# Optimization experiments

Hardware: AMD Instinct MI355X
Metric: run time of the kernel (lower is better)

## Reference

```python
import jax, jax.numpy as jnp
import numpy as np

B, FIN, N, K, FOUT = 8, 64, 2048, 20, 128
BN_EPS = 1e-5
LEAKY_SLOPE = 0.01


def _conv2d(x, w, b):
    # x: [B,C,H,W], w: [O,I,kh,kw] -> valid conv, stride 1
    y = jax.lax.conv_general_dilated(
        x, w, window_strides=(1, 1), padding='VALID',
        dimension_numbers=('NCHW', 'OIHW', 'NCHW'))
    return y + b[None, :, None, None]


def _batchnorm(x, gamma, beta):
    # training-mode BN: batch stats over (B,H,W), biased variance (torch default)
    mean = jnp.mean(x, axis=(0, 2, 3), keepdims=True)
    var = jnp.var(x, axis=(0, 2, 3), keepdims=True)
    xn = (x - mean) * jax.lax.rsqrt(var + BN_EPS)
    return xn * gamma[None, :, None, None] + beta[None, :, None, None]


def _edge_features(x, k):
    # x: [B, D, N] -> [B, 2D, N, k]
    xt = jnp.transpose(x, (0, 2, 1))                      # [B,N,D]
    sq = jnp.sum(xt * xt, axis=-1)                        # [B,N]
    dist = sq[:, :, None] + sq[:, None, :] - 2.0 * jnp.einsum('bnd,bmd->bnm', xt, xt)
    # smallest k+1 distances (self is the smallest); drop self
    _, idx = jax.lax.top_k(-dist, k + 1)                  # [B,N,k+1]
    idx = idx[:, :, 1:]                                   # [B,N,k]
    nb = jax.vmap(lambda pts, ind: pts[ind])(xt, idx)     # [B,N,k,D]
    neighbors = jnp.transpose(nb, (0, 3, 1, 2))           # [B,D,N,k]
    central = x[:, :, :, None]                            # [B,D,N,1]
    central_k = jnp.broadcast_to(central, neighbors.shape)
    return jnp.concatenate([central_k, neighbors - central], axis=1)


def setup_inputs() -> dict:
    key = jax.random.key(0)
    ks = jax.random.split(key, 4)
    x = jax.random.normal(ks[0], (B, FIN, N), dtype=jnp.float32)
    conv1_w = jax.random.normal(ks[1], (4 * FIN, 2 * FIN, 1, K // 2 + 1), dtype=jnp.float32) * 0.02
    conv1_b = jnp.zeros((4 * FIN,), jnp.float32)
    bn1_g = jnp.ones((4 * FIN,), jnp.float32)
    bn1_b = jnp.zeros((4 * FIN,), jnp.float32)
    conv2_w = jax.random.normal(ks[2], (2 * FOUT, 2 * FIN, 1, 2 * K), dtype=jnp.float32) * 0.02
    conv2_b = jnp.zeros((2 * FOUT,), jnp.float32)
    bn2_g = jnp.ones((2 * FOUT,), jnp.float32)
    bn2_b = jnp.zeros((2 * FOUT,), jnp.float32)
    return {"x": x, "conv1_w": conv1_w, "conv1_b": conv1_b, "bn1_g": bn1_g,
            "bn1_b": bn1_b, "conv2_w": conv2_w, "conv2_b": conv2_b,
            "bn2_g": bn2_g, "bn2_b": bn2_b, "k": K}


def reference(x, conv1_w, conv1_b, bn1_g, bn1_b, conv2_w, conv2_b, bn2_g, bn2_b, k):
    ee = _edge_features(x, k)                             # [B,2Fin,N,k]
    Bb, CC, NN, KK = ee.shape
    # inte_conv_hk: conv [1, k//2+1] -> [B,4Fin,N,k/2], BN, LeakyReLU
    h = _batchnorm(_conv2d(ee, conv1_w, conv1_b), bn1_g, bn1_b)
    h = jnp.where(h > 0, h, LEAKY_SLOPE * h)
    # transpose/view dance: [B,N,4Fin,k/2] -> [B,N,2Fin,k] -> [B,2Fin,N,k]
    inte = jnp.transpose(h, (0, 2, 1, 3)).reshape(Bb, NN, CC, KK)
    inte = jnp.transpose(inte, (0, 2, 1, 3))
    merge = jnp.concatenate([ee, inte], axis=3)           # [B,2Fin,N,2k]
    y = _batchnorm(_conv2d(merge, conv2_w, conv2_b), bn2_g, bn2_b)
    y = jax.nn.relu(y)                                    # [B,2Fout,N,1]
    fout = y.shape[1] // 2
    return y.reshape(Bb, fout, 2 * NN)                    # [B,Fout,2N]
```

## Files before the change

### kernel.cpp

```cpp
#include <hip/hip_runtime.h>
#include <stdint.h>

typedef unsigned int uint;
typedef unsigned short ushort;
typedef __attribute__((ext_vector_type(8))) short short8;
typedef __attribute__((ext_vector_type(4))) float f32x4;

__device__ __forceinline__ uint f2bf(float f) {
  uint u = __float_as_uint(f);
  return (u + 0x7fffu + ((u >> 16) & 1u)) >> 16;
}
__device__ __forceinline__ float bf2f(uint us) {
  return __uint_as_float(us << 16);
}
__device__ __forceinline__ uint cvtpk_bf16(float lo, float hi) {
  uint r;
  asm("v_cvt_pk_bf16_f32 %0, %1, %2" : "=v"(r) : "v"(lo), "v"(hi));
  return r;
}
__device__ __forceinline__ int lt_count(unsigned long long m) {
  return (int)__builtin_amdgcn_mbcnt_hi((uint)(m >> 32),
             __builtin_amdgcn_mbcnt_lo((uint)m, 0u));
}

__global__ __launch_bounds__(256) void prep_transpose(
    const float* __restrict__ w1, const float* __restrict__ w2,
    ushort* __restrict__ wp1, ushort* __restrict__ wpack,
    const float* __restrict__ x, uint* __restrict__ xtu,
    float* __restrict__ xtf, float* __restrict__ sqf) {
  __shared__ float t[64][65];
  int tid = threadIdx.x;
  if (blockIdx.x >= 256) {
    int g = (blockIdx.x - 256) * 256 + tid;
    if (g < 196608) {
      int chunk = g >> 9;
      int r = g & 511;
      int lane = r >> 3, j = r & 7;
      int tks = chunk >> 4;
      int ctile = chunk & 15;
      int tt0 = tks >> 1, ks = tks & 1;
      int c = ctile * 16 + (lane & 15);
      int d = ks * 32 + ((lane >> 4) << 3) + j;
      float val;
      if (tt0 < 11) {
        val = w1[c * 1408 + (64 + d) * 11 + tt0];
      } else {
        float s = 0.f;
        for (int tt = 0; tt < 11; ++tt)
          s += w1[c * 1408 + d * 11 + tt] - w1[c * 1408 + (64 + d) * 11 + tt];
        val = s;
      }
      wp1[g] = (ushort)f2bf(val);
    } else {
      int gp = g - 196608;
      int chunk = gp >> 9;
      int r = gp & 511;
      int lane = r >> 3, j = r & 7;
      int kb = chunk >> 5;
      int rem = chunk & 31;
      int ks = rem >> 4, ctile = rem & 15;
      int c = ctile * 16 + (lane & 15);
      int k = kb * 64 + ks * 32 + ((lane >> 4) << 3) + j;
      float val;
      if (k < 64) {
        int d = k;
        float s = 0.f;
        for (int jn = 0; jn < 20; ++jn)
          s += w2[c * 5120 + d * 40 + jn] - w2[c * 5120 + (64 + d) * 40 + jn];
        val = s;
      } else if (k < 1344) {
        int q = k - 64; int jn = q >> 6, d = q & 63;
        val = w2[c * 5120 + (64 + d) * 40 + jn];
      } else {
        int q = k - 1344; int ci = q / 20, jj = q - ci * 20;
        val = w2[c * 5120 + ci * 40 + 20 + jj];
      }
      wpack[gp] = (ushort)f2bf(val);
    }
    return;
  }
  int blk = blockIdx.x;
  int b = blk >> 5, n0 = (blk & 31) << 6;
  const float* xb = x + b * 131072;
  #pragma unroll
  for (int it = 0; it < 16; ++it) {
    int d = (it << 2) + (tid >> 6);
    int n = tid & 63;
    t[d][n] = xb[d * 2048 + n0 + n];
  }
  __syncthreads();
  #pragma unroll
  for (int it = 0; it < 8; ++it) {
    int n = (it << 3) + (tid >> 5);
    int dp = tid & 31;
    float f0 = t[2 * dp][n], f1 = t[2 * dp + 1][n];
    uint v = f2bf(f0) | (f2bf(f1) << 16);
    size_t col = (size_t)(b * 2048 + n0 + n);
    xtu[col * 32 + dp] = v;
    float2 fv; fv.x = f0; fv.y = f1;
    *(float2*)&xtf[(col << 6) + 2 * dp] = fv;
    float s = f0 * f0 + f1 * f1;
    #pragma unroll
    for (int off = 16; off > 0; off >>= 1) s += __shfl_xor(s, off);
    if (dp == 0) sqf[col] = s;
  }
}

__global__ __launch_bounds__(1024) void knn_kernel(
    const ushort* __restrict__ xbf_t, const float* __restrict__ sqf,
    int* __restrict__ cbuf) {
  __shared__ uint dist[16][1040];
  __shared__ uint surv[16][132];
  int tid = threadIdx.x;
  int wv = tid >> 6, lane = tid & 63;
  int grp = blockIdx.x >> 1;
  int half = blockIdx.x & 1;
  int cbase = half << 10;
  int row0 = grp << 4;
  int b = row0 >> 11, n0 = row0 & 2047;
  const ushort* xt = xbf_t + ((size_t)b << 17);
  const float* sqb = sqf + (b << 11);
  int m = lane & 15, quad = lane >> 4;
  short8 afr0 = *(const short8*)(xt + ((size_t)(n0 + m) << 6) + quad * 8);
  short8 afr1 = *(const short8*)(xt + ((size_t)(n0 + m) << 6) + 32 + quad * 8);
  for (int t = 0; t < 4; ++t) {
    int lcol = (((wv << 2) + t) << 4) + m;
    int col = cbase + lcol;
    short8 bfr0 = *(const short8*)(xt + ((size_t)col << 6) + quad * 8);
    short8 bfr1 = *(const short8*)(xt + ((size_t)col << 6) + 32 + quad * 8);
    f32x4 c = {};
    c = __builtin_amdgcn_mfma_f32_16x16x32_bf16(afr0, bfr0, c, 0, 0, 0);
    c = __builtin_amdgcn_mfma_f32_16x16x32_bf16(afr1, bfr1, c, 0, 0, 0);
    float sq = sqb[col];
    #pragma unroll
    for (int r = 0; r < 4; ++r) {
      float f = sq - 2.f * c[r];
      uint u = __float_as_uint(f);
      uint srt = u ^ ((uint)((int)u >> 31) | 0x80000000u);
      dist[quad * 4 + r][lcol] = (srt & 0xFFFFF800u) | (uint)col;
    }
  }
  __syncthreads();
  uint* dr = dist[wv];
  int selfl = (n0 + wv) - cbase;
  if (selfl >= 0 && selfl < 1024 && ((selfl & 63) == lane))
    dr[selfl] = 0xFFFFFFFFu;

  uint key[16];
  uint v0 = 0xFFFFFFFFu;
  #pragma unroll
  for (int l = 0; l < 16; ++l) {
    uint v = dr[(l << 6) + lane];
    key[l] = v;
    v0 = v0 < v ? v0 : v;
  }

  uint s = v0;
  #pragma unroll
  for (int k = 2; k <= 64; k <<= 1) {
    #pragma unroll
    for (int j = k >> 1; j > 0; j >>= 1) {
      uint o = (uint)__shfl_xor((int)s, j);
      bool up = ((lane & k) == 0);
      bool lower = ((lane & j) == 0);
      uint mn = s < o ? s : o;
      uint mx = s < o ? o : s;
      s = (lower == up) ? mn : mx;
    }
  }
  uint T = (uint)__shfl((int)s, 31);

  int base = 0;
  #pragma unroll
  for (int l = 0; l < 16; ++l) {
    uint v = key[l];
    bool f = (v <= T);
    unsigned long long mk = __ballot(f);
    if (f) {
      int pos = base + lt_count(mk);
      if (pos < 128) surv[wv][pos] = v;
    }
    base += __popcll(mk);
  }
  int S = base < 128 ? base : 128;
  if (lane < 4) surv[wv][S + lane] = 0xFFFFFFFFu;

  int outb = (row0 + wv) * 64 + (half << 5);
  uint k0 = (lane < S) ? surv[wv][lane] : 0xFFFFFFFFu;
  int r0 = 0;
  if (S > 64) {
    uint k1 = (lane + 64 < S) ? surv[wv][lane + 64] : 0xFFFFFFFFu;
    int r1 = 0;
    for (int i = 0; i < S; i += 4) {
      uint4 q = *(const uint4*)&surv[wv][i];
      r0 += (q.x < k0) + (q.y < k0) + (q.z < k0) + (q.w < k0);
      r1 += (q.x < k1) + (q.y < k1) + (q.z < k1) + (q.w < k1);
    }
    if (lane + 64 < S && r1 < 32) cbuf[outb + r1] = (int)(k1 & 2047u);
  } else {
    for (int i = 0; i < S; i += 4) {
      uint4 q = *(const uint4*)&surv[wv][i];
      r0 += (q.x < k0) + (q.y < k0) + (q.z < k0) + (q.w < k0);
    }
  }
  if (lane < S && r0 < 32) cbuf[outb + r0] = (int)(k0 & 2047u);
}

__global__ __launch_bounds__(256) void knn_merge(
    const float* __restrict__ xtf, const int* __restrict__ cbuf,
    int* __restrict__ idxout) {
  __shared__ double dkey[4][64];
  __shared__ int ccol[4][64];
  int tid = threadIdx.x;
  int wv = tid >> 6, lane = tid & 63;
  int row = (blockIdx.x << 2) + wv;
  int b = row >> 11, n = row & 2047;
  int ci = cbuf[row * 64 + lane];
  const float* xc = xtf + ((size_t)b << 17);
  const float4* xj4 = (const float4*)(xc + ((size_t)ci << 6));
  const float4* xi4 = (const float4*)(xc + ((size_t)n << 6));
  double dt = 0.0, s2 = 0.0;
  #pragma unroll 4
  for (int d4 = 0; d4 < 16; ++d4) {
    float4 vj = xj4[d4];
    float4 vi = xi4[d4];
    double a0 = (double)vj.x, a1 = (double)vj.y, a2 = (double)vj.z, a3 = (double)vj.w;
    s2 += a0 * a0 + a1 * a1 + a2 * a2 + a3 * a3;
    dt += (double)vi.x * a0 + (double)vi.y * a1 + (double)vi.z * a2 + (double)vi.w * a3;
  }
  dkey[wv][lane] = s2 - 2.0 * dt;
  ccol[wv][lane] = ci;
  __syncthreads();
  double kl = dkey[wv][lane];
  int rank = 0;
  for (int mm = 0; mm < 64; ++mm) {
    double km = dkey[wv][mm];
    int cm = ccol[wv][mm];
    if (km < kl || (km == kl && cm < ci)) ++rank;
  }
  if (rank < 20) idxout[row * 20 + rank] = ci;
}

__global__ __launch_bounds__(512, 4) void conv1_mfma(
    const ushort* __restrict__ xbf_t, const int* __restrict__ idxbuf,
    const ushort* __restrict__ wp1, uint* __restrict__ hu,
    float* __restrict__ stats) {
  __shared__ ushort sl[21][8][16][8];
  __shared__ int nidx[16][20];
  int tid = threadIdx.x;
  int p0 = blockIdx.x << 4;
  int b = p0 >> 11, n0 = p0 & 2047;
  const ushort* xt = xbf_t + ((size_t)b << 17);
  for (int v = tid; v < 320; v += 512) {
    int p = v / 20, j = v - p * 20;
    nidx[p][j] = idxbuf[(p0 + p) * 20 + j];
  }
  __syncthreads();
  for (int v = tid; v < 2688; v += 512) {
    int s = v >> 7;
    int r = v & 127;
    int p = r >> 3, i = r & 7;
    int col = (s == 0) ? (n0 + p) : nidx[p][s - 1];
    *(short8*)&sl[s][i][p ^ i][0] =
        *(const short8*)(xt + ((size_t)col << 6) + (i << 3));
  }
  __syncthreads();
  int lane = tid & 63, wave = tid >> 6;
  int m = lane & 15, quad = lane >> 4;
  #pragma unroll 1
  for (int pass = 0; pass < 2; ++pass) {
    int ctile = (pass << 3) + wave;
    int c = ctile * 16 + m;
    f32x4 acc[10] = {};
    f32x4 cacc = {};
    #pragma unroll 1
    for (int ks = 0; ks < 2; ++ks) {
      int cch = ks * 4 + quad;
      int ms = m ^ cch;
      short8 tb[11];
      #pragma unroll
      for (int t = 0; t < 11; ++t)
        tb[t] = *(const short8*)(wp1 + (((t * 2 + ks) * 16 + ctile) << 9) + lane * 8);
      short8 ub = *(const short8*)(wp1 + (((22 + ks) * 16 + ctile) << 9) + lane * 8);
      {
        short8 a = *(const short8*)&sl[0][cch][ms][0];
        cacc = __builtin_amdgcn_mfma_f32_16x16x32_bf16(a, ub, cacc, 0, 0, 0);
      }
      #pragma unroll
      for (int s = 1; s <= 20; ++s) {
        short8 a = *(const short8*)&sl[s][cch][ms][0];
        #pragma unroll
        for (int t = 0; t < 11; ++t) {
          int ko = s - 1 - t;
          if (ko >= 0 && ko < 10)
            acc[ko] = __builtin_amdgcn_mfma_f32_16x16x32_bf16(a, tb[t], acc[ko], 0, 0, 0);
        }
      }
    }
    float sacc = 0.f, ssacc = 0.f;
    #pragma unroll
    for (int r = 0; r < 4; ++r) {
      int p = (quad << 2) + r;
      int base5 = ((p0 + p) * 256 + c) * 5;
      float cc = cacc[r];
      #pragma unroll
      for (int q = 0; q < 5; ++q) {
        float f0 = acc[2 * q][r] + cc;
        float f1 = acc[2 * q + 1][r] + cc;
        sacc += f0 + f1;
        ssacc += f0 * f0 + f1 * f1;
        hu[base5 + q] = cvtpk_bf16(f0, f1);
      }
    }
    sacc += __shfl_xor(sacc, 16);  sacc += __shfl_xor(sacc, 32);
    ssacc += __shfl_xor(ssacc, 16); ssacc += __shfl_xor(ssacc, 32);
    if (quad == 0) {
      atomicAdd(&stats[c], sacc);
      atomicAdd(&stats[256 + c], ssacc);
    }
  }
}

__global__ __launch_bounds__(512, 4) void conv2_mfma(
    const ushort* __restrict__ xbf_t, const int* __restrict__ idxbuf,
    const uint* __restrict__ hu, const float* __restrict__ stats1,
    const float* __restrict__ g1, const float* __restrict__ be1,
    const ushort* __restrict__ wpack, float* __restrict__ yraw,
    float* __restrict__ stats) {
  __shared__ ushort As[2][4][64][64];
  __shared__ int nidx[64][20];
  __shared__ float cfA[257], cfB[257];
  int tid = threadIdx.x;
  int nblk = blockIdx.x & 1;
  int p0 = (blockIdx.x >> 1) << 6;
  int b = p0 >> 11, n0 = p0 & 2047;
  const ushort* xt = xbf_t + ((size_t)b << 17);

  if (tid < 256) {
    float mm = stats1[tid] * (1.f / 163840.f);
    float var = stats1[256 + tid] * (1.f / 163840.f) - mm * mm;
    float a = g1[tid] * rsqrtf(var + 1e-5f);
    cfA[tid] = a;
    cfB[tid] = be1[tid] - mm * a;
    if (tid == 0) { cfA[256] = 0.f; cfB[256] = 0.f; }
  }
  for (int v = tid; v < 1280; v += 512) {
    int p = v / 20, j = v - p * 20;
    nidx[p][j] = idxbuf[(p0 + p) * 20 + j];
  }
  __syncthreads();

  int pp = tid >> 3;
  int t7 = tid & 7;
  int off = t7 << 3;
  int wroff = ((t7 ^ (pp & 7)) << 3);

  auto build = [&](int phase, int buf) {
    int kb0 = phase << 2;
    short8 xv[4];
    uint4 hv[4];
    #pragma unroll
    for (int kc = 0; kc < 4; ++kc) {
      int kb = kb0 + kc;
      if (kb >= 61) continue;
      if (kb < 21) {
        int col = (kb == 0) ? (n0 + pp) : nidx[pp][kb - 1];
        xv[kc] = *(const short8*)(xt + ((size_t)col << 6) + off);
      } else {
        int q0 = (kb - 21) * 64 + off;
        hv[kc] = *(const uint4*)(hu + (size_t)(p0 + pp) * 1280 + (q0 >> 1));
      }
    }
    #pragma unroll
    for (int kc = 0; kc < 4; ++kc) {
      int kb = kb0 + kc;
      if (kb >= 61) continue;
      if (kb < 21) {
        *(short8*)&As[buf][kc][pp][wroff] = xv[kc];
      } else {
        int q0 = (kb - 21) * 64 + off;
        uint4 hvv = hv[kc];
        float f[8];
        f[0] = bf2f(hvv.x & 0xffffu); f[1] = bf2f(hvv.x >> 16);
        f[2] = bf2f(hvv.y & 0xffffu); f[3] = bf2f(hvv.y >> 16);
        f[4] = bf2f(hvv.z & 0xffffu); f[5] = bf2f(hvv.z >> 16);
        f[6] = bf2f(hvv.w & 0xffffu); f[7] = bf2f(hvv.w >> 16);
        int ch0 = q0 / 10;
        int rem = q0 - ch0 * 10;
        float a0 = cfA[ch0], b0 = cfB[ch0];
        float a1 = cfA[ch0 + 1], b1 = cfB[ch0 + 1];
        uint4 wv4;
        uint rr[4];
        #pragma unroll
        for (int i = 0; i < 4; ++i) {
          bool hlo = (rem + 2 * i) >= 10;
          bool hhi = (rem + 2 * i + 1) >= 10;
          float vlo = f[2 * i]     * (hlo ? a1 : a0) + (hlo ? b1 : b0);
          float vhi = f[2 * i + 1] * (hhi ? a1 : a0) + (hhi ? b1 : b0);
          vlo = fmaxf(vlo, 0.01f * vlo);
          vhi = fmaxf(vhi, 0.01f * vhi);
          rr[i] = cvtpk_bf16(vlo, vhi);
        }
        wv4.x = rr[0]; wv4.y = rr[1]; wv4.z = rr[2]; wv4.w = rr[3];
        *(uint4*)&As[buf][kc][pp][wroff] = wv4;
      }
    }
  };

  int lane = tid & 63, wave = tid >> 6;
  int m = lane & 15, quad = lane >> 4;
  int rdoff0 = ((quad ^ (m & 7)) << 3);
  int rdoff1 = (((4 + quad) ^ (m & 7)) << 3);
  f32x4 acc[4] = {};

  build(0, 0);
  __syncthreads();
  for (int phase = 0; phase < 16; ++phase) {
    int buf = phase & 1;
    if (phase < 15) build(phase + 1, buf ^ 1);
    #pragma unroll
    for (int kc = 0; kc < 4; ++kc) {
      int kb = (phase << 2) + kc;
      if (kb >= 61) break;
      #pragma unroll
      for (int ks = 0; ks < 2; ++ks) {
        int rdoff = ks ? rdoff1 : rdoff0;
        short8 afr[4];
        #pragma unroll
        for (int mt = 0; mt < 4; ++mt)
          afr[mt] = *(const short8*)&As[buf][kc][mt * 16 + m][rdoff];
        const ushort* bp = wpack +
            (((size_t)((kb * 2 + ks) * 16 + (nblk << 3) + wave)) << 9) + lane * 8;
        short8 bfr = *(const short8*)bp;
        #pragma unroll
        for (int mt = 0; mt < 4; ++mt)
          acc[mt] = __builtin_amdgcn_mfma_f32_16x16x32_bf16(afr[mt], bfr, acc[mt], 0, 0, 0);
      }
    }
    __syncthreads();
  }
  {
    int col = (nblk << 7) + (wave << 4) + m;
    float sacc = 0.f, ssacc = 0.f;
    #pragma unroll
    for (int mt = 0; mt < 4; ++mt) {
      #pragma unroll
      for (int r = 0; r < 4; ++r) {
        int prow = mt * 16 + quad * 4 + r;
        float v = acc[mt][r];
        sacc += v; ssacc += v * v;
        yraw[(size_t)(p0 + prow) * 256 + col] = v;
      }
    }
    sacc += __shfl_xor(sacc, 16);  sacc += __shfl_xor(sacc, 32);
    ssacc += __shfl_xor(ssacc, 16); ssacc += __shfl_xor(ssacc, 32);
    if (quad == 0) {
      atomicAdd(&stats[col], sacc);
      atomicAdd(&stats[256 + col], ssacc);
    }
  }
}

__global__ __launch_bounds__(256) void out_kernel(const float* __restrict__ yraw,
                                                  const float* __restrict__ stats2,
                                                  const float* __restrict__ g2,
                                                  const float* __restrict__ be2,
                                                  float* __restrict__ out) {
  __shared__ float t[64][257];
  __shared__ float c2A[256], c2B[256];
  int tid = threadIdx.x;
  int blk = blockIdx.x;
  int b = blk >> 5, n0 = (blk & 31) << 6;
  {
    float mm = stats2[tid] * (1.f / 16384.f);
    float var = stats2[256 + tid] * (1.f / 16384.f) - mm * mm;
    float a = g2[tid] * rsqrtf(var + 1e-5f);
    c2A[tid] = a;
    c2B[tid] = be2[tid] - mm * a;
  }
  for (int it = 0; it < 64; ++it)
    t[it][tid] = yraw[(b * 2048 + n0 + it) * 256 + tid];
  __syncthreads();
  int nsub4 = (tid & 15) << 2;
  int cq = tid >> 4;
  for (int it = 0; it < 16; ++it) {
    int c = (it << 4) + cq;
    float a = c2A[c], be = c2B[c];
    float4 v;
    v.x = a * t[nsub4 + 0][c] + be;
    v.y = a * t[nsub4 + 1][c] + be;
    v.z = a * t[nsub4 + 2][c] + be;
    v.w = a * t[nsub4 + 3][c] + be;
    v.x = v.x > 0.f ? v.x : 0.f;
    v.y = v.y > 0.f ? v.y : 0.f;
    v.z = v.z > 0.f ? v.z : 0.f;
    v.w = v.w > 0.f ? v.w : 0.f;
    *(float4*)&out[(size_t)(b * 256 + c) * 2048 + n0 + nsub4] = v;
  }
}

extern "C" void kernel_launch(void* const* d_in, const int* in_sizes, int n_in,
                              void* d_out, int out_size, void* d_ws, size_t ws_size,
                              hipStream_t stream) {
  const float* x   = (const float*)d_in[0];
  const float* w1  = (const float*)d_in[1];
  const float* g1  = (const float*)d_in[3];
  const float* be1 = (const float*)d_in[4];
  const float* w2  = (const float*)d_in[5];
  const float* g2  = (const float*)d_in[7];
  const float* be2 = (const float*)d_in[8];
  float* out = (float*)d_out;
  char* w = (char*)d_ws;
  float* sqf    = (float*)(w);
  int*  idxbuf  = (int*)(w + 131072);
  uint* hu      = (uint*)(w + 1441792);
  float* xtf    = (float*)(w + 1441792);
  int*  cbuf    = (int*)(w + 9830400);
  float* yraw   = (float*)(w + 85327872);
  float* stats  = (float*)(w + 102105088);
  ushort* wp1   = (ushort*)(w + 102113280);
  ushort* wpack = (ushort*)(w + 102506496);
  ushort* xbf_t = (ushort*)(w + 104505344);

  hipMemsetAsync(stats, 0, 4096, stream);
  prep_transpose<<<4928, 256, 0, stream>>>(w1, w2, wp1, wpack,
                                           x, (uint*)xbf_t, xtf, sqf);
  knn_kernel<<<2048, 1024, 0, stream>>>(xbf_t, sqf, cbuf);
  knn_merge<<<4096, 256, 0, stream>>>(xtf, cbuf, idxbuf);
  conv1_mfma<<<1024, 512, 0, stream>>>(xbf_t, idxbuf, wp1, hu, stats);
  conv2_mfma<<<512, 512, 0, stream>>>(xbf_t, idxbuf, hu, stats, g1, be1,
                                      wpack, yraw, stats + 512);
  out_kernel<<<256, 256, 0, stream>>>(yraw, stats + 512, g2, be2, out);
}
```

Before: 289.9 us.

## Store conv2 output channel-major and simplify out kernel; vectorize knn key loads

conv2 now writes its raw output in [B,C,N] order with 16-byte vector stores, so the BN2+ReLU output kernel becomes a flat elementwise pass with no shared-memory transpose and runs on more blocks. The knn kernel masks the self-distance while writing the key to shared memory, dropping a separate fix-up step. Each lane then reads four contiguous keys with one vector load, which changes which candidates each lane holds; this is valid only if the later selection does not rely on the old strided assignment. The main cost targeted is the transpose and bandwidth of the final kernel.

```diff
diff --git a/kernel.cpp b/kernel.cpp
--- a/kernel.cpp
+++ b/kernel.cpp
@@ -134,25 +134,29 @@
     float sq = sqb[col];
     #pragma unroll
     for (int r = 0; r < 4; ++r) {
+      int drow = quad * 4 + r;
       float f = sq - 2.f * c[r];
       uint u = __float_as_uint(f);
       uint srt = u ^ ((uint)((int)u >> 31) | 0x80000000u);
-      dist[quad * 4 + r][lcol] = (srt & 0xFFFFF800u) | (uint)col;
+      uint keyv = (srt & 0xFFFFF800u) | (uint)col;
+      if (col == n0 + drow) keyv = 0xFFFFFFFFu;
+      dist[drow][lcol] = keyv;
     }
   }
   __syncthreads();
   uint* dr = dist[wv];
-  int selfl = (n0 + wv) - cbase;
-  if (selfl >= 0 && selfl < 1024 && ((selfl & 63) == lane))
-    dr[selfl] = 0xFFFFFFFFu;
 
   uint key[16];
   uint v0 = 0xFFFFFFFFu;
   #pragma unroll
-  for (int l = 0; l < 16; ++l) {
-    uint v = dr[(l << 6) + lane];
-    key[l] = v;
-    v0 = v0 < v ? v0 : v;
+  for (int l = 0; l < 4; ++l) {
+    uint4 q = *(const uint4*)&dr[(l << 8) + (lane << 2)];
+    key[4 * l + 0] = q.x; key[4 * l + 1] = q.y;
+    key[4 * l + 2] = q.z; key[4 * l + 3] = q.w;
+    uint m0 = q.x < q.y ? q.x : q.y;
+    uint m1 = q.z < q.w ? q.z : q.w;
+    m0 = m0 < m1 ? m0 : m1;
+    v0 = v0 < m0 ? v0 : m0;
   }
 
   uint s = v0;
@@ -325,7 +329,7 @@
     const ushort* __restrict__ xbf_t, const int* __restrict__ idxbuf,
     const uint* __restrict__ hu, const float* __restrict__ stats1,
     const float* __restrict__ g1, const float* __restrict__ be1,
-    const ushort* __restrict__ wpack, float* __restrict__ yraw,
+    const ushort* __restrict__ wpack, float* __restrict__ yrawT,
     float* __restrict__ stats) {
   __shared__ ushort As[2][4][64][64];
   __shared__ int nidx[64][20];
@@ -444,13 +448,10 @@
     float sacc = 0.f, ssacc = 0.f;
     #pragma unroll
     for (int mt = 0; mt < 4; ++mt) {
-      #pragma unroll
-      for (int r = 0; r < 4; ++r) {
-        int prow = mt * 16 + quad * 4 + r;
-        float v = acc[mt][r];
-        sacc += v; ssacc += v * v;
-        yraw[(size_t)(p0 + prow) * 256 + col] = v;
-      }
+      f32x4 v4 = acc[mt];
+      sacc += v4[0] + v4[1] + v4[2] + v4[3];
+      ssacc += v4[0] * v4[0] + v4[1] * v4[1] + v4[2] * v4[2] + v4[3] * v4[3];
+      *(f32x4*)&yrawT[(((size_t)(b << 8) + col) << 11) + n0 + mt * 16 + quad * 4] = v4;
     }
     sacc += __shfl_xor(sacc, 16);  sacc += __shfl_xor(sacc, 32);
     ssacc += __shfl_xor(ssacc, 16); ssacc += __shfl_xor(ssacc, 32);
@@ -461,16 +462,13 @@
   }
 }
 
-__global__ __launch_bounds__(256) void out_kernel(const float* __restrict__ yraw,
+__global__ __launch_bounds__(256) void out_kernel(const float* __restrict__ yrawT,
                                                   const float* __restrict__ stats2,
                                                   const float* __restrict__ g2,
                                                   const float* __restrict__ be2,
                                                   float* __restrict__ out) {
-  __shared__ float t[64][257];
   __shared__ float c2A[256], c2B[256];
   int tid = threadIdx.x;
-  int blk = blockIdx.x;
-  int b = blk >> 5, n0 = (blk & 31) << 6;
   {
     float mm = stats2[tid] * (1.f / 16384.f);
     float var = stats2[256 + tid] * (1.f / 16384.f) - mm * mm;
@@ -478,24 +476,20 @@
     c2A[tid] = a;
     c2B[tid] = be2[tid] - mm * a;
   }
-  for (int it = 0; it < 64; ++it)
-    t[it][tid] = yraw[(b * 2048 + n0 + it) * 256 + tid];
-  __syncthreads();
-  int nsub4 = (tid & 15) << 2;
-  int cq = tid >> 4;
-  for (int it = 0; it < 16; ++it) {
-    int c = (it << 4) + cq;
+  __syncthreads();
+  #pragma unroll
+  for (int it = 0; it < 4; ++it) {
+    size_t i4 = (size_t)blockIdx.x * 1024 + it * 256 + tid;
+    int c = (int)((i4 >> 9) & 255);
     float a = c2A[c], be = c2B[c];
-    float4 v;
-    v.x = a * t[nsub4 + 0][c] + be;
-    v.y = a * t[nsub4 + 1][c] + be;
-    v.z = a * t[nsub4 + 2][c] + be;
-    v.w = a * t[nsub4 + 3][c] + be;
-    v.x = v.x > 0.f ? v.x : 0.f;
-    v.y = v.y > 0.f ? v.y : 0.f;
-    v.z = v.z > 0.f ? v.z : 0.f;
-    v.w = v.w > 0.f ? v.w : 0.f;
-    *(float4*)&out[(size_t)(b * 256 + c) * 2048 + n0 + nsub4] = v;
+    float4 v = *(const float4*)&yrawT[i4 << 2];
+    float t0 = a * v.x + be, t1 = a * v.y + be;
+    float t2 = a * v.z + be, t3 = a * v.w + be;
+    v.x = t0 > 0.f ? t0 : 0.f;
+    v.y = t1 > 0.f ? t1 : 0.f;
+    v.z = t2 > 0.f ? t2 : 0.f;
+    v.w = t3 > 0.f ? t3 : 0.f;
+    *(float4*)&out[i4 << 2] = v;
   }
 }
 
@@ -530,5 +524,5 @@
   conv1_mfma<<<1024, 512, 0, stream>>>(xbf_t, idxbuf, wp1, hu, stats);
   conv2_mfma<<<512, 512, 0, stream>>>(xbf_t, idxbuf, hu, stats, g1, be1,
                                       wpack, yraw, stats + 512);
-  out_kernel<<<256, 256, 0, stream>>>(yraw, stats + 512, g2, be2, out);
-}
+  out_kernel<<<1024, 256, 0, stream>>>(yraw, stats + 512, g2, be2, out);
+}
```

After: 293.2 us. No clear change (+1.1%).

## Merge conv2 output-channel halves into one 1024-thread block per point tile

Applied to the files above, without the earlier changes.

Before, two 512-thread blocks each covered one half of the 256 output channels for the same 64-point tile, and each block built the full gathered A tile (neighbor features plus BN1/LeakyReLU-applied inte features). The change launches 256 blocks of 1024 threads (16 waves) so each block covers all 256 channels, and the A tile is built once with each thread loading 4 elements instead of 8. This removes the duplicated gather and BN1 activation work, but halves the grid to 256 blocks, which is about one block per CU, and may reduce occupancy and latency hiding. Launch bounds of 1024 threads also tighten the per-thread register budget.

```diff
diff --git a/kernel.cpp b/kernel.cpp
--- a/kernel.cpp
+++ b/kernel.cpp
@@ -321,7 +321,7 @@
   }
 }
 
-__global__ __launch_bounds__(512, 4) void conv2_mfma(
+__global__ __launch_bounds__(1024, 4) void conv2_mfma(
     const ushort* __restrict__ xbf_t, const int* __restrict__ idxbuf,
     const uint* __restrict__ hu, const float* __restrict__ stats1,
     const float* __restrict__ g1, const float* __restrict__ be1,
@@ -331,8 +331,7 @@
   __shared__ int nidx[64][20];
   __shared__ float cfA[257], cfB[257];
   int tid = threadIdx.x;
-  int nblk = blockIdx.x & 1;
-  int p0 = (blockIdx.x >> 1) << 6;
+  int p0 = blockIdx.x << 6;
   int b = p0 >> 11, n0 = p0 & 2047;
   const ushort* xt = xbf_t + ((size_t)b << 17);
 
@@ -344,31 +343,31 @@
     cfB[tid] = be1[tid] - mm * a;
     if (tid == 0) { cfA[256] = 0.f; cfB[256] = 0.f; }
   }
-  for (int v = tid; v < 1280; v += 512) {
+  for (int v = tid; v < 1280; v += 1024) {
     int p = v / 20, j = v - p * 20;
     nidx[p][j] = idxbuf[(p0 + p) * 20 + j];
   }
   __syncthreads();
 
-  int pp = tid >> 3;
-  int t7 = tid & 7;
-  int off = t7 << 3;
-  int wroff = ((t7 ^ (pp & 7)) << 3);
+  int pp = tid >> 4;
+  int t15 = tid & 15;
+  int off = t15 << 2;
+  int wroff = ((((t15 >> 1) ^ (pp & 7)) << 3) | ((t15 & 1) << 2));
 
   auto build = [&](int phase, int buf) {
     int kb0 = phase << 2;
-    short8 xv[4];
-    uint4 hv[4];
+    short4 xv[4];
+    uint2 hv[4];
     #pragma unroll
     for (int kc = 0; kc < 4; ++kc) {
       int kb = kb0 + kc;
       if (kb >= 61) continue;
       if (kb < 21) {
         int col = (kb == 0) ? (n0 + pp) : nidx[pp][kb - 1];
-        xv[kc] = *(const short8*)(xt + ((size_t)col << 6) + off);
+        xv[kc] = *(const short4*)(xt + ((size_t)col << 6) + off);
       } else {
         int q0 = (kb - 21) * 64 + off;
-        hv[kc] = *(const uint4*)(hu + (size_t)(p0 + pp) * 1280 + (q0 >> 1));
+        hv[kc] = *(const uint2*)(hu + (size_t)(p0 + pp) * 1280 + (q0 >> 1));
       }
     }
     #pragma unroll
@@ -376,33 +375,30 @@
       int kb = kb0 + kc;
       if (kb >= 61) continue;
       if (kb < 21) {
-        *(short8*)&As[buf][kc][pp][wroff] = xv[kc];
+        *(short4*)&As[buf][kc][pp][wroff] = xv[kc];
       } else {
         int q0 = (kb - 21) * 64 + off;
-        uint4 hvv = hv[kc];
-        float f[8];
-        f[0] = bf2f(hvv.x & 0xffffu); f[1] = bf2f(hvv.x >> 16);
-        f[2] = bf2f(hvv.y & 0xffffu); f[3] = bf2f(hvv.y >> 16);
-        f[4] = bf2f(hvv.z & 0xffffu); f[5] = bf2f(hvv.z >> 16);
-        f[6] = bf2f(hvv.w & 0xffffu); f[7] = bf2f(hvv.w >> 16);
+        uint2 hvv = hv[kc];
+        float f0 = bf2f(hvv.x & 0xffffu), f1 = bf2f(hvv.x >> 16);
+        float f2 = bf2f(hvv.y & 0xffffu), f3 = bf2f(hvv.y >> 16);
         int ch0 = q0 / 10;
         int rem = q0 - ch0 * 10;
         float a0 = cfA[ch0], b0 = cfB[ch0];
         float a1 = cfA[ch0 + 1], b1 = cfB[ch0 + 1];
-        uint4 wv4;
-        uint rr[4];
-        #pragma unroll
-        for (int i = 0; i < 4; ++i) {
-          bool hlo = (rem + 2 * i) >= 10;
-          bool hhi = (rem + 2 * i + 1) >= 10;
-          float vlo = f[2 * i]     * (hlo ? a1 : a0) + (hlo ? b1 : b0);
-          float vhi = f[2 * i + 1] * (hhi ? a1 : a0) + (hhi ? b1 : b0);
-          vlo = fmaxf(vlo, 0.01f * vlo);
-          vhi = fmaxf(vhi, 0.01f * vhi);
-          rr[i] = cvtpk_bf16(vlo, vhi);
-        }
-        wv4.x = rr[0]; wv4.y = rr[1]; wv4.z = rr[2]; wv4.w = rr[3];
-        *(uint4*)&As[buf][kc][pp][wroff] = wv4;
+        bool h0 = (rem + 0) >= 10, h1 = (rem + 1) >= 10;
+        bool h2 = (rem + 2) >= 10, h3 = (rem + 3) >= 10;
+        float v0 = f0 * (h0 ? a1 : a0) + (h0 ? b1 : b0);
+        float v1 = f1 * (h1 ? a1 : a0) + (h1 ? b1 : b0);
+        float v2 = f2 * (h2 ? a1 : a0) + (h2 ? b1 : b0);
+        float v3 = f3 * (h3 ? a1 : a0) + (h3 ? b1 : b0);
+        v0 = fmaxf(v0, 0.01f * v0);
+        v1 = fmaxf(v1, 0.01f * v1);
+        v2 = fmaxf(v2, 0.01f * v2);
+        v3 = fmaxf(v3, 0.01f * v3);
+        uint2 wv2;
+        wv2.x = cvtpk_bf16(v0, v1);
+        wv2.y = cvtpk_bf16(v2, v3);
+        *(uint2*)&As[buf][kc][pp][wroff] = wv2;
       }
     }
   };
@@ -430,7 +426,7 @@
         for (int mt = 0; mt < 4; ++mt)
           afr[mt] = *(const short8*)&As[buf][kc][mt * 16 + m][rdoff];
         const ushort* bp = wpack +
-            (((size_t)((kb * 2 + ks) * 16 + (nblk << 3) + wave)) << 9) + lane * 8;
+            (((size_t)((kb * 2 + ks) * 16 + wave)) << 9) + lane * 8;
         short8 bfr = *(const short8*)bp;
         #pragma unroll
         for (int mt = 0; mt < 4; ++mt)
@@ -440,7 +436,7 @@
     __syncthreads();
   }
   {
-    int col = (nblk << 7) + (wave << 4) + m;
+    int col = (wave << 4) + m;
     float sacc = 0.f, ssacc = 0.f;
     #pragma unroll
     for (int mt = 0; mt < 4; ++mt) {
@@ -528,7 +524,7 @@
   knn_kernel<<<2048, 1024, 0, stream>>>(xbf_t, sqf, cbuf);
   knn_merge<<<4096, 256, 0, stream>>>(xtf, cbuf, idxbuf);
   conv1_mfma<<<1024, 512, 0, stream>>>(xbf_t, idxbuf, wp1, hu, stats);
-  conv2_mfma<<<512, 512, 0, stream>>>(xbf_t, idxbuf, hu, stats, g1, be1,
-                                      wpack, yraw, stats + 512);
+  conv2_mfma<<<256, 1024, 0, stream>>>(xbf_t, idxbuf, hu, stats, g1, be1,
+                                       wpack, yraw, stats + 512);
   out_kernel<<<256, 256, 0, stream>>>(yraw, stats + 512, g2, be2, out);
 }
```

New measurement: 285.8 us, median of 2. Within noise of the previous version (-1.4%).
